# Optimization experiments

Hardware: AMD Instinct MI355X
Metric: run time of the kernel (lower is better)

Reference implementation:

```python
import jax, jax.numpy as jnp
import numpy as np

N_NODES = 100000
N_EDGES = 1600000
DIM = 128
N_BUNDLES = 8
BUNDLE_DIM = 4
HIDDEN = 256
TIME = 2


def setup_inputs() -> dict:
    key = jax.random.key(0)
    ks = jax.random.split(key, 8)
    x = jax.random.normal(ks[0], (N_NODES, DIM), dtype=jnp.float32)
    node_rep = jax.random.normal(ks[1], (N_NODES, N_BUNDLES, BUNDLE_DIM, BUNDLE_DIM), dtype=jnp.float32)
    # edge list; ensure every node has out-degree >= 1 so degree norm is finite
    src_extra = jax.random.randint(ks[2], (N_EDGES - N_NODES,), 0, N_NODES)
    src = jnp.concatenate([jnp.arange(N_NODES), src_extra]).astype(jnp.int64)
    dst = jax.random.randint(ks[3], (N_EDGES,), 0, N_NODES).astype(jnp.int64)
    w1 = jax.random.normal(ks[4], (HIDDEN, DIM), dtype=jnp.float32) * (1.0 / np.sqrt(DIM))
    b1 = jnp.zeros((HIDDEN,), dtype=jnp.float32)
    w2 = jax.random.normal(ks[5], (DIM, HIDDEN), dtype=jnp.float32) * (1.0 / np.sqrt(HIDDEN))
    b2 = jnp.zeros((DIM,), dtype=jnp.float32)
    return {"x": x, "node_rep": node_rep, "src": src, "dst": dst,
            "w1": w1, "b1": b1, "w2": w2, "b2": b2}


def reference(x, node_rep, src, dst, w1, b1, w2, b2):
    n = x.shape[0]
    # out-degrees (number of edges with node as source)
    deg = jax.ops.segment_sum(jnp.ones_like(src, dtype=x.dtype), src, num_segments=n)
    # u_mul_v: per-edge product of src and dst degrees -> symmetric norm coefs
    norm_coefs = jax.lax.rsqrt(deg[src] * deg[dst])  # [E]
    # per-bundle rotation: einsum('abcd,abde->abce', node_rep, vf)
    vf = x.reshape(n, N_BUNDLES, BUNDLE_DIM, -1)
    vf = jnp.einsum('nbcd,nbde->nbce', node_rep, vf)
    h = vf.reshape(n, DIM)
    # u_mul_e_sum repeated `time` times: out[dst] += h[src] * coef
    for _ in range(TIME):
        h = jax.ops.segment_sum(h[src] * norm_coefs[:, None], dst, num_segments=n)
    # inverse rotation with transposed node_rep
    vf = h.reshape(n, N_BUNDLES, BUNDLE_DIM, -1)
    vf = jnp.einsum('nbdc,nbde->nbce', node_rep, vf)
    h = vf.reshape(n, DIM)
    # feed-forward (dropout=0, exact GELU as in torch nn.GELU default)
    h = jax.nn.gelu(h @ w1.T + b1, approximate=False)
    return h @ w2.T + b2
```

## Files before the change

kernel.cpp:

```cpp
#include <hip/hip_runtime.h>
#include <hip/hip_bf16.h>
#include <math.h>

#define DIM 128
#define HID 256

typedef short s8x __attribute__((ext_vector_type(8)));
typedef float f4x __attribute__((ext_vector_type(4)));

__device__ __forceinline__ unsigned short f2bf(float f) {
    unsigned int u = __float_as_uint(f);
    u += 0x7FFF + ((u >> 16) & 1);
    return (unsigned short)(u >> 16);
}
__device__ __forceinline__ float bf2f(unsigned short b) {
    return __uint_as_float(((unsigned int)b) << 16);
}
__device__ __forceinline__ float bflo(unsigned int p) {
    return __uint_as_float(p << 16);
}
__device__ __forceinline__ float bfhi(unsigned int p) {
    return __uint_as_float(p & 0xffff0000u);
}


__global__ __launch_bounds__(256) void hist_kernel(
        const int* __restrict__ src, const int* __restrict__ dst,
        int* __restrict__ TD, int* __restrict__ TS, int nE, int nbuck, int chunk) {
    __shared__ int hd[1024], hs[1024];
    const int tid = threadIdx.x, blk = blockIdx.x;
    for (int b = tid; b < nbuck; b += 256) { hd[b] = 0; hs[b] = 0; }
    __syncthreads();
    int beg = blk * chunk, end = min(beg + chunk, nE);
    for (int i = beg + tid; i < end; i += 256) {
        atomicAdd(&hd[dst[i] >> 7], 1);
        atomicAdd(&hs[src[i] >> 7], 1);
    }
    __syncthreads();
    for (int b = tid; b < nbuck; b += 256) {
        TD[b * 256 + blk] = hd[b];
        TS[b * 256 + blk] = hs[b];
    }
}

__global__ void scan_blocks(const int* in, int* out, int* bsums, int n) {
    __shared__ int part[256];
    const int tid = threadIdx.x;
    const int base = blockIdx.x * 1024 + tid * 4;
    int v[4];
    int sum = 0;
#pragma unroll
    for (int k = 0; k < 4; ++k) {
        v[k] = (base + k < n) ? in[base + k] : 0;
        sum += v[k];
    }
    part[tid] = sum;
    __syncthreads();
    for (int off = 1; off < 256; off <<= 1) {
        int t = (tid >= off) ? part[tid - off] : 0;
        __syncthreads();
        part[tid] += t;
        __syncthreads();
    }
    int excl = part[tid] - sum;
    if (tid == 255) bsums[blockIdx.x] = part[255];
#pragma unroll
    for (int k = 0; k < 4; ++k) {
        if (base + k < n) out[base + k] = excl;
        excl += v[k];
    }
}

__global__ void scan_sums(int* bsums, int nb) {
    __shared__ int part[256];
    const int tid = threadIdx.x;
    const int base = tid * 4;
    int v[4];
    int sum = 0;
#pragma unroll
    for (int k = 0; k < 4; ++k) {
        v[k] = (base + k < nb) ? bsums[base + k] : 0;
        sum += v[k];
    }
    part[tid] = sum;
    __syncthreads();
    for (int off = 1; off < 256; off <<= 1) {
        int t = (tid >= off) ? part[tid - off] : 0;
        __syncthreads();
        part[tid] += t;
        __syncthreads();
    }
    int excl = part[tid] - sum;
#pragma unroll
    for (int k = 0; k < 4; ++k) {
        if (base + k < nb) bsums[base + k] = excl;
        excl += v[k];
    }
}

__global__ void scan_add(int* T, const int* __restrict__ bsums, int n2, int half, int E) {
    int i = blockIdx.x * blockDim.x + threadIdx.x;
    if (i < n2) {
        int v = T[i] + bsums[i >> 10];
        T[i] = (i >= half) ? v - E : v;
    }
}

__global__ __launch_bounds__(256) void scatter_edges(
        const int* __restrict__ src, const int* __restrict__ dst,
        const int* __restrict__ TD, const int* __restrict__ TS,
        unsigned long long* __restrict__ pairs, int* __restrict__ srcval,
        int nE, int nbuck, int chunk) {
    __shared__ int cd[1024], cs[1024];
    const int tid = threadIdx.x, blk = blockIdx.x;
    for (int b = tid; b < nbuck; b += 256) {
        cd[b] = TD[b * 256 + blk];
        cs[b] = TS[b * 256 + blk];
    }
    __syncthreads();
    int beg = blk * chunk, end = min(beg + chunk, nE);
    for (int i = beg + tid; i < end; i += 256) {
        int s = src[i], d = dst[i];
        int pd = atomicAdd(&cd[d >> 7], 1);
        pairs[pd] = ((unsigned long long)(unsigned)s << 32) | (unsigned)d;
        int ps = atomicAdd(&cs[s >> 7], 1);
        srcval[ps] = s;
    }
}

__global__ __launch_bounds__(256) void finalize_kernel(
        const unsigned long long* __restrict__ pairs, const int* __restrict__ TD,
        const int* __restrict__ srcval, const int* __restrict__ TS,
        int* __restrict__ rowstart, int* __restrict__ esrc,
        float* __restrict__ rdeg, int nE, int nbuck, int nN) {
    __shared__ int hist[128], sbuf[128], cur[128];
    const int tid = threadIdx.x, b = blockIdx.x;
    int beg = TD[b * 256];
    int end = (b + 1 < nbuck) ? TD[(b + 1) * 256] : nE;
    if (tid < 128) hist[tid] = 0;
    __syncthreads();
    for (int i = beg + tid; i < end; i += 256)
        atomicAdd(&hist[(int)((unsigned)pairs[i] & 127u)], 1);
    __syncthreads();
    int v = (tid < 128) ? hist[tid] : 0;
    if (tid < 128) sbuf[tid] = v;
    __syncthreads();
    for (int off = 1; off < 128; off <<= 1) {
        int t = (tid < 128 && tid >= off) ? sbuf[tid - off] : 0;
        __syncthreads();
        if (tid < 128) sbuf[tid] += t;
        __syncthreads();
    }
    if (tid < 128) {
        int excl = sbuf[tid] - v;
        cur[tid] = excl;
        int idx = (b << 7) + tid;
        if (idx <= nN) rowstart[idx] = beg + excl;
    }
    __syncthreads();
    for (int i = beg + tid; i < end; i += 256) {
        unsigned long long p = pairs[i];
        int l = (int)((unsigned)p & 127u);
        int s = (int)(p >> 32);
        int pos = atomicAdd(&cur[l], 1);
        esrc[beg + pos] = s;
    }
    __syncthreads();
    if (tid < 128) hist[tid] = 0;
    __syncthreads();
    int beg2 = TS[b * 256];
    int end2 = (b + 1 < nbuck) ? TS[(b + 1) * 256] : nE;
    for (int i = beg2 + tid; i < end2; i += 256)
        atomicAdd(&hist[srcval[i] & 127], 1);
    __syncthreads();
    if (tid < 128) {
        int idx = (b << 7) + tid;
        if (idx < nN) rdeg[idx] = rsqrtf((float)hist[tid]);
    }
}

__global__ void rot_cvt_kernel(const float* __restrict__ x, const float* __restrict__ R,
                               unsigned short* __restrict__ h0,
                               const float* __restrict__ w1, const float* __restrict__ w2,
                               unsigned short* __restrict__ w1b, unsigned short* __restrict__ w2b,
                               int n, int nbRot) {
    if ((int)blockIdx.x >= nbRot) {
        int t = (blockIdx.x - nbRot) * 256 + threadIdx.x;
        for (int i = t; i < 32768; i += 4096) {
            w1b[i] = f2bf(w1[i]);
            w2b[i] = f2bf(w2[i]);
        }
        return;
    }
    int u = blockIdx.x * blockDim.x + threadIdx.x;
    if (u >= n * 8) return;
    int nd = u >> 3, b = u & 7;
    const float* xp = &x[(size_t)nd * DIM + b * 16];
    const float* Rp = &R[(size_t)nd * DIM + b * 16];
    float xv[16], rv[16];
#pragma unroll
    for (int d = 0; d < 4; ++d) {
        *(float4*)&xv[d * 4] = *(const float4*)&xp[d * 4];
        *(float4*)&rv[d * 4] = *(const float4*)&Rp[d * 4];
    }
    unsigned short ob[16];
#pragma unroll
    for (int c = 0; c < 4; ++c)
#pragma unroll
        for (int e = 0; e < 4; ++e) {
            float acc = 0.f;
#pragma unroll
            for (int d = 0; d < 4; ++d) acc += rv[c * 4 + d] * xv[d * 4 + e];
            ob[c * 4 + e] = f2bf(acc);
        }
    unsigned short* op = &h0[(size_t)nd * DIM + b * 16];
    *(s8x*)&op[0] = *(s8x*)&ob[0];
    *(s8x*)&op[8] = *(s8x*)&ob[8];
}

__global__ __launch_bounds__(256) void gather_kernel(
        const unsigned short* __restrict__ hsrc, const int* __restrict__ esrc,
        const float* __restrict__ rdeg, const int* __restrict__ rowstart,
        unsigned short* __restrict__ hdst, int n) {
    int node = blockIdx.x * 8 + (threadIdx.x >> 5);
    int lane = threadIdx.x & 31;
    if (node >= n) return;
    int beg = rowstart[node];
    int end = rowstart[node + 1];
    float rd = rdeg[node];
    float a0 = 0.f, a1 = 0.f, a2 = 0.f, a3 = 0.f;
    int i = beg;
    for (; i + 2 <= end; i += 2) {
        int s0 = esrc[i], s1 = esrc[i + 1];
        float c0 = rdeg[s0] * rd;
        float c1 = rdeg[s1] * rd;
        uint2 p0 = *(const uint2*)&hsrc[(size_t)s0 * DIM + lane * 4];
        uint2 p1 = *(const uint2*)&hsrc[(size_t)s1 * DIM + lane * 4];
        a0 += bflo(p0.x) * c0 + bflo(p1.x) * c1;
        a1 += bfhi(p0.x) * c0 + bfhi(p1.x) * c1;
        a2 += bflo(p0.y) * c0 + bflo(p1.y) * c1;
        a3 += bfhi(p0.y) * c0 + bfhi(p1.y) * c1;
    }
    if (i < end) {
        int s0 = esrc[i];
        float c0 = rdeg[s0] * rd;
        uint2 p0 = *(const uint2*)&hsrc[(size_t)s0 * DIM + lane * 4];
        a0 += bflo(p0.x) * c0;
        a1 += bfhi(p0.x) * c0;
        a2 += bflo(p0.y) * c0;
        a3 += bfhi(p0.y) * c0;
    }
    uint2 packed;
    packed.x = (unsigned int)f2bf(a0) | ((unsigned int)f2bf(a1) << 16);
    packed.y = (unsigned int)f2bf(a2) | ((unsigned int)f2bf(a3) << 16);
    *(uint2*)&hdst[(size_t)node * DIM + lane * 4] = packed;
}

#define ABST 136
#define HBST 264
__global__ __launch_bounds__(256, 3) void ffn_kernel(
        const unsigned short* __restrict__ h,
        const float* __restrict__ R,
        const unsigned short* __restrict__ w1b,
        const float* __restrict__ b1,
        const unsigned short* __restrict__ w2b,
        const float* __restrict__ b2,
        float* __restrict__ out, int n) {
    __shared__ unsigned short abuf[64 * ABST];
    __shared__ unsigned short hbuf[64 * HBST];
    const int tid  = threadIdx.x;
    const int node0 = blockIdx.x * 64;
    const int wave = tid >> 6;
    const int lane = tid & 63;
    const int lr = lane & 15;
    const int lq = lane >> 4;

    for (int u = tid; u < 512; u += 256) {
        int nd = u >> 3, b = u & 7;
        int gn = node0 + nd;
        float hv[16], rv[16];
        if (gn < n) {
            const unsigned short* hp = &h[(size_t)gn * DIM + b * 16];
            const float* Rp = &R[(size_t)gn * DIM + b * 16];
            unsigned short hraw[16];
            *(s8x*)&hraw[0] = *(const s8x*)&hp[0];
            *(s8x*)&hraw[8] = *(const s8x*)&hp[8];
#pragma unroll
            for (int d = 0; d < 16; ++d) hv[d] = bf2f(hraw[d]);
#pragma unroll
            for (int d = 0; d < 4; ++d)
                *(float4*)&rv[d * 4] = *(const float4*)&Rp[d * 4];
        } else {
#pragma unroll
            for (int d = 0; d < 16; ++d) { hv[d] = 0.f; rv[d] = 0.f; }
        }
#pragma unroll
        for (int c = 0; c < 4; ++c) {
            unsigned short gb[4];
#pragma unroll
            for (int e = 0; e < 4; ++e) {
                float acc = 0.f;
#pragma unroll
                for (int d = 0; d < 4; ++d) acc += rv[d * 4 + c] * hv[d * 4 + e];
                gb[e] = f2bf(acc);
            }
            *(ushort4*)&abuf[nd * ABST + b * 16 + c * 4] =
                make_ushort4(gb[0], gb[1], gb[2], gb[3]);
        }
    }
    __syncthreads();

    f4x acc1[4][4];
#pragma unroll
    for (int mt = 0; mt < 4; ++mt)
#pragma unroll
        for (int nt = 0; nt < 4; ++nt) acc1[mt][nt] = (f4x){0.f, 0.f, 0.f, 0.f};

    const int nw = wave * 64;
    for (int ks = 0; ks < 4; ++ks) {
        const int k0 = ks * 32 + lq * 8;
        s8x af[4], bf[4];
#pragma unroll
        for (int mt = 0; mt < 4; ++mt)
            af[mt] = *(const s8x*)&abuf[(mt * 16 + lr) * ABST + k0];
#pragma unroll
        for (int nt = 0; nt < 4; ++nt)
            bf[nt] = *(const s8x*)&w1b[(size_t)(nw + nt * 16 + lr) * 128 + k0];
#pragma unroll
        for (int mt = 0; mt < 4; ++mt)
#pragma unroll
            for (int nt = 0; nt < 4; ++nt)
                acc1[mt][nt] = __builtin_amdgcn_mfma_f32_16x16x32_bf16(
                    af[mt], bf[nt], acc1[mt][nt], 0, 0, 0);
    }
#pragma unroll
    for (int nt = 0; nt < 4; ++nt) {
        int nn = nw + nt * 16 + lr;
        float bias = b1[nn];
#pragma unroll
        for (int mt = 0; mt < 4; ++mt) {
#pragma unroll
            for (int r = 0; r < 4; ++r) {
                float v = acc1[mt][nt][r] + bias;
                v = 0.5f * v * (1.f + erff(v * 0.70710678118654752f));
                hbuf[(mt * 16 + lq * 4 + r) * HBST + nn] = f2bf(v);
            }
        }
    }
    __syncthreads();

    f4x acc2[4][2];
#pragma unroll
    for (int mt = 0; mt < 4; ++mt)
#pragma unroll
        for (int nt = 0; nt < 2; ++nt) acc2[mt][nt] = (f4x){0.f, 0.f, 0.f, 0.f};

    const int nw2 = wave * 32;
    for (int ks = 0; ks < 8; ++ks) {
        const int k0 = ks * 32 + lq * 8;
        s8x af[4], bf2v[2];
#pragma unroll
        for (int mt = 0; mt < 4; ++mt)
            af[mt] = *(const s8x*)&hbuf[(mt * 16 + lr) * HBST + k0];
#pragma unroll
        for (int nt = 0; nt < 2; ++nt)
            bf2v[nt] = *(const s8x*)&w2b[(size_t)(nw2 + nt * 16 + lr) * 256 + k0];
#pragma unroll
        for (int mt = 0; mt < 4; ++mt)
#pragma unroll
            for (int nt = 0; nt < 2; ++nt)
                acc2[mt][nt] = __builtin_amdgcn_mfma_f32_16x16x32_bf16(
                    af[mt], bf2v[nt], acc2[mt][nt], 0, 0, 0);
    }
#pragma unroll
    for (int nt = 0; nt < 2; ++nt) {
        int n2 = nw2 + nt * 16 + lr;
        float bias = b2[n2];
#pragma unroll
        for (int mt = 0; mt < 4; ++mt) {
#pragma unroll
            for (int r = 0; r < 4; ++r) {
                int gn = node0 + mt * 16 + lq * 4 + r;
                if (gn < n) out[(size_t)gn * DIM + n2] = acc2[mt][nt][r] + bias;
            }
        }
    }
}

extern "C" void kernel_launch(void* const* d_in, const int* in_sizes, int n_in,
                              void* d_out, int out_size, void* d_ws, size_t ws_size,
                              hipStream_t stream) {
    const float* x   = (const float*)d_in[0];
    const float* R   = (const float*)d_in[1];
    const int*   src = (const int*)d_in[2];
    const int*   dst = (const int*)d_in[3];
    const float* w1  = (const float*)d_in[4];
    const float* b1  = (const float*)d_in[5];
    const float* w2  = (const float*)d_in[6];
    const float* b2  = (const float*)d_in[7];
    float* out = (float*)d_out;

    const int N = in_sizes[0] / DIM;
    const int E = in_sizes[2];

    const int nbuck = (N + 127) >> 7;
    const int chunk = (E + 255) / 256;
    const int nScan = nbuck * 256;
    const int nScan2 = 2 * nScan;
    const int nbScan2 = (nScan2 + 1023) / 1024;

    unsigned short* hA = (unsigned short*)d_ws;
    unsigned short* hM = hA + (size_t)N * DIM;
    unsigned long long* pairs = (unsigned long long*)hM;
    int* srcval = (int*)(pairs + E);
    float* rdeg     = (float*)(hM + (size_t)N * DIM);
    int*   rowstart = (int*)(rdeg + N);
    int*   esrc     = rowstart + (N + 1);
    int*   TD       = esrc + E;
    int*   TS       = TD + nScan;
    int*   bsums    = TS + nScan;
    unsigned short* w1b = (unsigned short*)(bsums + 1024);
    unsigned short* w2b = w1b + 32768;

    const int BLK = 256;

    hist_kernel<<<256, BLK, 0, stream>>>(src, dst, TD, TS, E, nbuck, chunk);
    scan_blocks<<<nbScan2, BLK, 0, stream>>>(TD, TD, bsums, nScan2);
    scan_sums<<<1, BLK, 0, stream>>>(bsums, nbScan2);
    scan_add<<<(nScan2 + BLK - 1) / BLK, BLK, 0, stream>>>(TD, bsums, nScan2, nScan, E);
    scatter_edges<<<256, BLK, 0, stream>>>(src, dst, TD, TS, pairs, srcval, E, nbuck, chunk);
    finalize_kernel<<<nbuck, BLK, 0, stream>>>(pairs, TD, srcval, TS, rowstart, esrc, rdeg, E, nbuck, N);

    const int nbRot = ((size_t)N * 8 + BLK - 1) / BLK;
    rot_cvt_kernel<<<nbRot + 16, BLK, 0, stream>>>(x, R, hA, w1, w2, w1b, w2b, N, nbRot);

    gather_kernel<<<(N + 7) / 8, BLK, 0, stream>>>(hA, esrc, rdeg, rowstart, hM, N);
    gather_kernel<<<(N + 7) / 8, BLK, 0, stream>>>(hM, esrc, rdeg, rowstart, hA, N);

    ffn_kernel<<<(N + 63) / 64, BLK, 0, stream>>>(hA, R, w1b, b1, w2b, b2, out, N);
}
```

Measured before the change: 444.0 us.

## Replace bucketed CSR build with atomic counting sort and pack edge coefficients

Replaces the two-level bucketed histogram/scatter/finalize CSR construction with per-node global atomic degree counts, one scan, and an atomic-cursor scatter. It also stores (src, precomputed norm coefficient) pairs per edge so the gather skips the rdeg lookup. The gather now uses 16 lanes per node with 16-byte loads, and the FFN shares one LDS buffer between its two stages to allow 4 blocks per CU. Global atomics on random node ids may contend, and the edge order within a row becomes nondeterministic.

New measurement: 554.2 us. 24.8% more time.

```diff
diff --git a/kernel.cpp b/kernel.cpp
--- a/kernel.cpp
+++ b/kernel.cpp
@@ -24,22 +24,22 @@
 }
 
 
-__global__ __launch_bounds__(256) void hist_kernel(
+__global__ void prep_kernel(const float* __restrict__ w1, const float* __restrict__ w2,
+                            unsigned short* __restrict__ w1b, unsigned short* __restrict__ w2b,
+                            int* __restrict__ outdeg, int* __restrict__ rowcnt, int nN) {
+    const int t = blockIdx.x * 256 + threadIdx.x;
+    w1b[t] = f2bf(w1[t]);
+    w2b[t] = f2bf(w2[t]);
+    for (int i = t; i < nN; i += 32768) { outdeg[i] = 0; rowcnt[i] = 0; }
+}
+
+__global__ __launch_bounds__(256) void count_kernel(
         const int* __restrict__ src, const int* __restrict__ dst,
-        int* __restrict__ TD, int* __restrict__ TS, int nE, int nbuck, int chunk) {
-    __shared__ int hd[1024], hs[1024];
-    const int tid = threadIdx.x, blk = blockIdx.x;
-    for (int b = tid; b < nbuck; b += 256) { hd[b] = 0; hs[b] = 0; }
-    __syncthreads();
-    int beg = blk * chunk, end = min(beg + chunk, nE);
-    for (int i = beg + tid; i < end; i += 256) {
-        atomicAdd(&hd[dst[i] >> 7], 1);
-        atomicAdd(&hs[src[i] >> 7], 1);
-    }
-    __syncthreads();
-    for (int b = tid; b < nbuck; b += 256) {
-        TD[b * 256 + blk] = hd[b];
-        TS[b * 256 + blk] = hs[b];
+        int* __restrict__ outdeg, int* __restrict__ rowcnt, int nE) {
+    int i = blockIdx.x * 256 + threadIdx.x;
+    if (i < nE) {
+        atomicAdd(&outdeg[src[i]], 1);
+        atomicAdd(&rowcnt[dst[i]], 1);
     }
 }
 
@@ -98,100 +98,37 @@
     }
 }
 
-__global__ void scan_add(int* T, const int* __restrict__ bsums, int n2, int half, int E) {
+__global__ void scan_add(int* __restrict__ rowstart, const int* __restrict__ bsums,
+                         int* __restrict__ cursor, const int* __restrict__ outdeg,
+                         float* __restrict__ rdeg, int nN, int E) {
     int i = blockIdx.x * blockDim.x + threadIdx.x;
-    if (i < n2) {
-        int v = T[i] + bsums[i >> 10];
-        T[i] = (i >= half) ? v - E : v;
-    }
-}
-
-__global__ __launch_bounds__(256) void scatter_edges(
+    if (i < nN) {
+        int v = rowstart[i] + bsums[i >> 10];
+        rowstart[i] = v;
+        cursor[i] = v;
+        rdeg[i] = rsqrtf((float)outdeg[i]);
+    }
+    if (i == 0) rowstart[nN] = E;
+}
+
+template<bool PACK>
+__global__ __launch_bounds__(256) void scatter_kernel(
         const int* __restrict__ src, const int* __restrict__ dst,
-        const int* __restrict__ TD, const int* __restrict__ TS,
-        unsigned long long* __restrict__ pairs, int* __restrict__ srcval,
-        int nE, int nbuck, int chunk) {
-    __shared__ int cd[1024], cs[1024];
-    const int tid = threadIdx.x, blk = blockIdx.x;
-    for (int b = tid; b < nbuck; b += 256) {
-        cd[b] = TD[b * 256 + blk];
-        cs[b] = TS[b * 256 + blk];
-    }
-    __syncthreads();
-    int beg = blk * chunk, end = min(beg + chunk, nE);
-    for (int i = beg + tid; i < end; i += 256) {
-        int s = src[i], d = dst[i];
-        int pd = atomicAdd(&cd[d >> 7], 1);
-        pairs[pd] = ((unsigned long long)(unsigned)s << 32) | (unsigned)d;
-        int ps = atomicAdd(&cs[s >> 7], 1);
-        srcval[ps] = s;
-    }
-}
-
-__global__ __launch_bounds__(256) void finalize_kernel(
-        const unsigned long long* __restrict__ pairs, const int* __restrict__ TD,
-        const int* __restrict__ srcval, const int* __restrict__ TS,
-        int* __restrict__ rowstart, int* __restrict__ esrc,
-        float* __restrict__ rdeg, int nE, int nbuck, int nN) {
-    __shared__ int hist[128], sbuf[128], cur[128];
-    const int tid = threadIdx.x, b = blockIdx.x;
-    int beg = TD[b * 256];
-    int end = (b + 1 < nbuck) ? TD[(b + 1) * 256] : nE;
-    if (tid < 128) hist[tid] = 0;
-    __syncthreads();
-    for (int i = beg + tid; i < end; i += 256)
-        atomicAdd(&hist[(int)((unsigned)pairs[i] & 127u)], 1);
-    __syncthreads();
-    int v = (tid < 128) ? hist[tid] : 0;
-    if (tid < 128) sbuf[tid] = v;
-    __syncthreads();
-    for (int off = 1; off < 128; off <<= 1) {
-        int t = (tid < 128 && tid >= off) ? sbuf[tid - off] : 0;
-        __syncthreads();
-        if (tid < 128) sbuf[tid] += t;
-        __syncthreads();
-    }
-    if (tid < 128) {
-        int excl = sbuf[tid] - v;
-        cur[tid] = excl;
-        int idx = (b << 7) + tid;
-        if (idx <= nN) rowstart[idx] = beg + excl;
-    }
-    __syncthreads();
-    for (int i = beg + tid; i < end; i += 256) {
-        unsigned long long p = pairs[i];
-        int l = (int)((unsigned)p & 127u);
-        int s = (int)(p >> 32);
-        int pos = atomicAdd(&cur[l], 1);
-        esrc[beg + pos] = s;
-    }
-    __syncthreads();
-    if (tid < 128) hist[tid] = 0;
-    __syncthreads();
-    int beg2 = TS[b * 256];
-    int end2 = (b + 1 < nbuck) ? TS[(b + 1) * 256] : nE;
-    for (int i = beg2 + tid; i < end2; i += 256)
-        atomicAdd(&hist[srcval[i] & 127], 1);
-    __syncthreads();
-    if (tid < 128) {
-        int idx = (b << 7) + tid;
-        if (idx < nN) rdeg[idx] = rsqrtf((float)hist[tid]);
+        int* __restrict__ cursor, const float* __restrict__ rdeg,
+        uint2* __restrict__ ecsr, int* __restrict__ esrcA, int nE) {
+    int i = blockIdx.x * 256 + threadIdx.x;
+    if (i >= nE) return;
+    int s = src[i], d = dst[i];
+    int pos = atomicAdd(&cursor[d], 1);
+    if (PACK) {
+        ecsr[pos] = make_uint2((unsigned)s, __float_as_uint(rdeg[s] * rdeg[d]));
+    } else {
+        esrcA[pos] = s;
     }
 }
 
 __global__ void rot_cvt_kernel(const float* __restrict__ x, const float* __restrict__ R,
-                               unsigned short* __restrict__ h0,
-                               const float* __restrict__ w1, const float* __restrict__ w2,
-                               unsigned short* __restrict__ w1b, unsigned short* __restrict__ w2b,
-                               int n, int nbRot) {
-    if ((int)blockIdx.x >= nbRot) {
-        int t = (blockIdx.x - nbRot) * 256 + threadIdx.x;
-        for (int i = t; i < 32768; i += 4096) {
-            w1b[i] = f2bf(w1[i]);
-            w2b[i] = f2bf(w2[i]);
-        }
-        return;
-    }
+                               unsigned short* __restrict__ h0, int n) {
     int u = blockIdx.x * blockDim.x + threadIdx.x;
     if (u >= n * 8) return;
     int nd = u >> 3, b = u & 7;
@@ -218,47 +155,75 @@
     *(s8x*)&op[8] = *(s8x*)&ob[8];
 }
 
+template<bool PACK>
 __global__ __launch_bounds__(256) void gather_kernel(
-        const unsigned short* __restrict__ hsrc, const int* __restrict__ esrc,
+        const unsigned short* __restrict__ hsrc,
+        const uint2* __restrict__ ecsr, const int* __restrict__ esrcA,
         const float* __restrict__ rdeg, const int* __restrict__ rowstart,
         unsigned short* __restrict__ hdst, int n) {
-    int node = blockIdx.x * 8 + (threadIdx.x >> 5);
-    int lane = threadIdx.x & 31;
+    const int node = blockIdx.x * 16 + (threadIdx.x >> 4);
+    const int lane = threadIdx.x & 15;
     if (node >= n) return;
-    int beg = rowstart[node];
-    int end = rowstart[node + 1];
-    float rd = rdeg[node];
+    const int beg = rowstart[node];
+    const int end = rowstart[node + 1];
+    float rd = 0.f;
+    if (!PACK) rd = rdeg[node];
     float a0 = 0.f, a1 = 0.f, a2 = 0.f, a3 = 0.f;
+    float a4 = 0.f, a5 = 0.f, a6 = 0.f, a7 = 0.f;
     int i = beg;
     for (; i + 2 <= end; i += 2) {
-        int s0 = esrc[i], s1 = esrc[i + 1];
-        float c0 = rdeg[s0] * rd;
-        float c1 = rdeg[s1] * rd;
-        uint2 p0 = *(const uint2*)&hsrc[(size_t)s0 * DIM + lane * 4];
-        uint2 p1 = *(const uint2*)&hsrc[(size_t)s1 * DIM + lane * 4];
+        int s0, s1;
+        float c0, c1;
+        if (PACK) {
+            uint2 e0 = ecsr[i], e1 = ecsr[i + 1];
+            s0 = (int)e0.x; c0 = __uint_as_float(e0.y);
+            s1 = (int)e1.x; c1 = __uint_as_float(e1.y);
+        } else {
+            s0 = esrcA[i]; s1 = esrcA[i + 1];
+            c0 = rdeg[s0] * rd; c1 = rdeg[s1] * rd;
+        }
+        uint4 p0 = *(const uint4*)&hsrc[(size_t)s0 * DIM + lane * 8];
+        uint4 p1 = *(const uint4*)&hsrc[(size_t)s1 * DIM + lane * 8];
         a0 += bflo(p0.x) * c0 + bflo(p1.x) * c1;
         a1 += bfhi(p0.x) * c0 + bfhi(p1.x) * c1;
         a2 += bflo(p0.y) * c0 + bflo(p1.y) * c1;
         a3 += bfhi(p0.y) * c0 + bfhi(p1.y) * c1;
+        a4 += bflo(p0.z) * c0 + bflo(p1.z) * c1;
+        a5 += bfhi(p0.z) * c0 + bfhi(p1.z) * c1;
+        a6 += bflo(p0.w) * c0 + bflo(p1.w) * c1;
+        a7 += bfhi(p0.w) * c0 + bfhi(p1.w) * c1;
     }
     if (i < end) {
-        int s0 = esrc[i];
-        float c0 = rdeg[s0] * rd;
-        uint2 p0 = *(const uint2*)&hsrc[(size_t)s0 * DIM + lane * 4];
+        int s0;
+        float c0;
+        if (PACK) {
+            uint2 e0 = ecsr[i];
+            s0 = (int)e0.x; c0 = __uint_as_float(e0.y);
+        } else {
+            s0 = esrcA[i];
+            c0 = rdeg[s0] * rd;
+        }
+        uint4 p0 = *(const uint4*)&hsrc[(size_t)s0 * DIM + lane * 8];
         a0 += bflo(p0.x) * c0;
         a1 += bfhi(p0.x) * c0;
         a2 += bflo(p0.y) * c0;
         a3 += bfhi(p0.y) * c0;
-    }
-    uint2 packed;
-    packed.x = (unsigned int)f2bf(a0) | ((unsigned int)f2bf(a1) << 16);
-    packed.y = (unsigned int)f2bf(a2) | ((unsigned int)f2bf(a3) << 16);
-    *(uint2*)&hdst[(size_t)node * DIM + lane * 4] = packed;
+        a4 += bflo(p0.z) * c0;
+        a5 += bfhi(p0.z) * c0;
+        a6 += bflo(p0.w) * c0;
+        a7 += bfhi(p0.w) * c0;
+    }
+    uint4 o;
+    o.x = (unsigned)f2bf(a0) | ((unsigned)f2bf(a1) << 16);
+    o.y = (unsigned)f2bf(a2) | ((unsigned)f2bf(a3) << 16);
+    o.z = (unsigned)f2bf(a4) | ((unsigned)f2bf(a5) << 16);
+    o.w = (unsigned)f2bf(a6) | ((unsigned)f2bf(a7) << 16);
+    *(uint4*)&hdst[(size_t)node * DIM + lane * 8] = o;
 }
 
 #define ABST 136
 #define HBST 264
-__global__ __launch_bounds__(256, 3) void ffn_kernel(
+__global__ __launch_bounds__(256, 4) void ffn_kernel(
         const unsigned short* __restrict__ h,
         const float* __restrict__ R,
         const unsigned short* __restrict__ w1b,
@@ -266,8 +231,9 @@
         const unsigned short* __restrict__ w2b,
         const float* __restrict__ b2,
         float* __restrict__ out, int n) {
-    __shared__ unsigned short abuf[64 * ABST];
-    __shared__ unsigned short hbuf[64 * HBST];
+    __shared__ unsigned short smem[64 * HBST];
+    unsigned short* abuf = smem;
+    unsigned short* hbuf = smem;
     const int tid  = threadIdx.x;
     const int node0 = blockIdx.x * 64;
     const int wave = tid >> 6;
@@ -319,20 +285,22 @@
     const int nw = wave * 64;
     for (int ks = 0; ks < 4; ++ks) {
         const int k0 = ks * 32 + lq * 8;
-        s8x af[4], bf[4];
+        s8x af[4], bfv[4];
 #pragma unroll
         for (int mt = 0; mt < 4; ++mt)
             af[mt] = *(const s8x*)&abuf[(mt * 16 + lr) * ABST + k0];
 #pragma unroll
         for (int nt = 0; nt < 4; ++nt)
-            bf[nt] = *(const s8x*)&w1b[(size_t)(nw + nt * 16 + lr) * 128 + k0];
+            bfv[nt] = *(const s8x*)&w1b[(size_t)(nw + nt * 16 + lr) * 128 + k0];
 #pragma unroll
         for (int mt = 0; mt < 4; ++mt)
 #pragma unroll
             for (int nt = 0; nt < 4; ++nt)
                 acc1[mt][nt] = __builtin_amdgcn_mfma_f32_16x16x32_bf16(
-                    af[mt], bf[nt], acc1[mt][nt], 0, 0, 0);
-    }
+                    af[mt], bfv[nt], acc1[mt][nt], 0, 0, 0);
+    }
+    __syncthreads();
+
 #pragma unroll
     for (int nt = 0; nt < 4; ++nt) {
         int nn = nw + nt * 16 + lr;
@@ -403,39 +371,61 @@
     const int N = in_sizes[0] / DIM;
     const int E = in_sizes[2];
 
-    const int nbuck = (N + 127) >> 7;
-    const int chunk = (E + 255) / 256;
-    const int nScan = nbuck * 256;
-    const int nScan2 = 2 * nScan;
-    const int nbScan2 = (nScan2 + 1023) / 1024;
-
     unsigned short* hA = (unsigned short*)d_ws;
     unsigned short* hM = hA + (size_t)N * DIM;
-    unsigned long long* pairs = (unsigned long long*)hM;
-    int* srcval = (int*)(pairs + E);
-    float* rdeg     = (float*)(hM + (size_t)N * DIM);
-    int*   rowstart = (int*)(rdeg + N);
-    int*   esrc     = rowstart + (N + 1);
-    int*   TD       = esrc + E;
-    int*   TS       = TD + nScan;
-    int*   bsums    = TS + nScan;
+    char* edge_base = (char*)(hM + (size_t)N * DIM);
+    const size_t tail_bytes = (size_t)N * 4 * 3 + (size_t)(N + 1) * 4 +
+                              1024 * 4 + 2 * 32768 * 2;
+    const size_t fixed_bytes = (size_t)N * DIM * 4;
+    const bool use_pack =
+        (fixed_bytes + (size_t)E * 8 + tail_bytes) <= ws_size;
+    const size_t edge_bytes = use_pack ? (size_t)E * 8 : (size_t)E * 4;
+
+    uint2* ecsr = (uint2*)edge_base;
+    int*   esrcA = (int*)edge_base;
+    char* q = edge_base + edge_bytes;
+    float* rdeg     = (float*)q;
+    int*   outdeg   = (int*)(rdeg + N);
+    int*   rowcnt   = outdeg + N;
+    int*   rowstart = rowcnt + N;
+    int*   bsums    = rowstart + (N + 1);
     unsigned short* w1b = (unsigned short*)(bsums + 1024);
     unsigned short* w2b = w1b + 32768;
+    int* cursor = rowcnt;
 
     const int BLK = 256;
-
-    hist_kernel<<<256, BLK, 0, stream>>>(src, dst, TD, TS, E, nbuck, chunk);
-    scan_blocks<<<nbScan2, BLK, 0, stream>>>(TD, TD, bsums, nScan2);
-    scan_sums<<<1, BLK, 0, stream>>>(bsums, nbScan2);
-    scan_add<<<(nScan2 + BLK - 1) / BLK, BLK, 0, stream>>>(TD, bsums, nScan2, nScan, E);
-    scatter_edges<<<256, BLK, 0, stream>>>(src, dst, TD, TS, pairs, srcval, E, nbuck, chunk);
-    finalize_kernel<<<nbuck, BLK, 0, stream>>>(pairs, TD, srcval, TS, rowstart, esrc, rdeg, E, nbuck, N);
+    const int nbScan = (N + 1023) / 1024;
+    const int nbE = (E + BLK - 1) / BLK;
+
+    prep_kernel<<<128, BLK, 0, stream>>>(w1, w2, w1b, w2b, outdeg, rowcnt, N);
+
+    count_kernel<<<nbE, BLK, 0, stream>>>(src, dst, outdeg, rowcnt, E);
+    scan_blocks<<<nbScan, BLK, 0, stream>>>(rowcnt, rowstart, bsums, N);
+    scan_sums<<<1, BLK, 0, stream>>>(bsums, nbScan);
+    scan_add<<<(N + BLK - 1) / BLK, BLK, 0, stream>>>(rowstart, bsums, cursor,
+                                                      outdeg, rdeg, N, E);
+    if (use_pack)
+        scatter_kernel<true><<<nbE, BLK, 0, stream>>>(src, dst, cursor, rdeg,
+                                                      ecsr, esrcA, E);
+    else
+        scatter_kernel<false><<<nbE, BLK, 0, stream>>>(src, dst, cursor, rdeg,
+                                                       ecsr, esrcA, E);
 
     const int nbRot = ((size_t)N * 8 + BLK - 1) / BLK;
-    rot_cvt_kernel<<<nbRot + 16, BLK, 0, stream>>>(x, R, hA, w1, w2, w1b, w2b, N, nbRot);
-
-    gather_kernel<<<(N + 7) / 8, BLK, 0, stream>>>(hA, esrc, rdeg, rowstart, hM, N);
-    gather_kernel<<<(N + 7) / 8, BLK, 0, stream>>>(hM, esrc, rdeg, rowstart, hA, N);
+    rot_cvt_kernel<<<nbRot, BLK, 0, stream>>>(x, R, hA, N);
+
+    const int nbG = (N + 15) / 16;
+    if (use_pack) {
+        gather_kernel<true><<<nbG, BLK, 0, stream>>>(hA, ecsr, esrcA, rdeg,
+                                                     rowstart, hM, N);
+        gather_kernel<true><<<nbG, BLK, 0, stream>>>(hM, ecsr, esrcA, rdeg,
+                                                     rowstart, hA, N);
+    } else {
+        gather_kernel<false><<<nbG, BLK, 0, stream>>>(hA, ecsr, esrcA, rdeg,
+                                                      rowstart, hM, N);
+        gather_kernel<false><<<nbG, BLK, 0, stream>>>(hM, ecsr, esrcA, rdeg,
+                                                      rowstart, hA, N);
+    }
 
     ffn_kernel<<<(N + 63) / 64, BLK, 0, stream>>>(hA, R, w1b, b1, w2b, b2, out, N);
 }
```

## Compact edge buffers, precompute edge coefficients, widen gather loads, shrink FFN LDS

Applied to the files above, without the earlier changes.

Scatter now writes 32-bit packed (src<<7|dst_lo) pairs and a single byte per source entry, where it used to write 64-bit pairs and 32-bit source values. The old finalize kernel is split into a source-degree pass and a destination CSR pass. When the workspace is large enough, that pass stores (src, coef) pairs so the gathers skip the random rdeg lookups. The gather uses 16 lanes per node with 16-byte loads, and the FFN kernel aliases its two LDS buffers (adding a barrier) so it can raise launch bounds to 4 blocks. This trades an extra kernel launch and 8-byte edge reads for less scattered traffic, and relies on the workspace-size check.

Result: faster. 430.7 us (-3.0%).

```diff
diff --git a/kernel.cpp b/kernel.cpp
--- a/kernel.cpp
+++ b/kernel.cpp
@@ -109,7 +109,7 @@
 __global__ __launch_bounds__(256) void scatter_edges(
         const int* __restrict__ src, const int* __restrict__ dst,
         const int* __restrict__ TD, const int* __restrict__ TS,
-        unsigned long long* __restrict__ pairs, int* __restrict__ srcval,
+        unsigned int* __restrict__ pairs, unsigned char* __restrict__ sbyte,
         int nE, int nbuck, int chunk) {
     __shared__ int cd[1024], cs[1024];
     const int tid = threadIdx.x, blk = blockIdx.x;
@@ -122,17 +122,36 @@
     for (int i = beg + tid; i < end; i += 256) {
         int s = src[i], d = dst[i];
         int pd = atomicAdd(&cd[d >> 7], 1);
-        pairs[pd] = ((unsigned long long)(unsigned)s << 32) | (unsigned)d;
+        pairs[pd] = ((unsigned)s << 7) | (unsigned)(d & 127);
         int ps = atomicAdd(&cs[s >> 7], 1);
-        srcval[ps] = s;
-    }
-}
-
-__global__ __launch_bounds__(256) void finalize_kernel(
-        const unsigned long long* __restrict__ pairs, const int* __restrict__ TD,
-        const int* __restrict__ srcval, const int* __restrict__ TS,
-        int* __restrict__ rowstart, int* __restrict__ esrc,
+        sbyte[ps] = (unsigned char)(s & 127);
+    }
+}
+
+__global__ __launch_bounds__(256) void finalize_src(
+        const unsigned char* __restrict__ sbyte, const int* __restrict__ TS,
         float* __restrict__ rdeg, int nE, int nbuck, int nN) {
+    __shared__ int hist[128];
+    const int tid = threadIdx.x, b = blockIdx.x;
+    if (tid < 128) hist[tid] = 0;
+    __syncthreads();
+    int beg = TS[b * 256];
+    int end = (b + 1 < nbuck) ? TS[(b + 1) * 256] : nE;
+    for (int i = beg + tid; i < end; i += 256)
+        atomicAdd(&hist[sbyte[i]], 1);
+    __syncthreads();
+    if (tid < 128) {
+        int idx = (b << 7) + tid;
+        if (idx < nN) rdeg[idx] = rsqrtf((float)hist[tid]);
+    }
+}
+
+template<bool PACK>
+__global__ __launch_bounds__(256) void finalize_dst(
+        const unsigned int* __restrict__ pairs, const int* __restrict__ TD,
+        const float* __restrict__ rdeg,
+        int* __restrict__ rowstart, uint2* __restrict__ ecsr,
+        int* __restrict__ esrcA, int nE, int nbuck, int nN) {
     __shared__ int hist[128], sbuf[128], cur[128];
     const int tid = threadIdx.x, b = blockIdx.x;
     int beg = TD[b * 256];
@@ -140,7 +159,7 @@
     if (tid < 128) hist[tid] = 0;
     __syncthreads();
     for (int i = beg + tid; i < end; i += 256)
-        atomicAdd(&hist[(int)((unsigned)pairs[i] & 127u)], 1);
+        atomicAdd(&hist[(int)(pairs[i] & 127u)], 1);
     __syncthreads();
     int v = (tid < 128) ? hist[tid] : 0;
     if (tid < 128) sbuf[tid] = v;
@@ -159,23 +178,16 @@
     }
     __syncthreads();
     for (int i = beg + tid; i < end; i += 256) {
-        unsigned long long p = pairs[i];
-        int l = (int)((unsigned)p & 127u);
-        int s = (int)(p >> 32);
+        unsigned int p = pairs[i];
+        int l = (int)(p & 127u);
+        int s = (int)(p >> 7);
         int pos = atomicAdd(&cur[l], 1);
-        esrc[beg + pos] = s;
-    }
-    __syncthreads();
-    if (tid < 128) hist[tid] = 0;
-    __syncthreads();
-    int beg2 = TS[b * 256];
-    int end2 = (b + 1 < nbuck) ? TS[(b + 1) * 256] : nE;
-    for (int i = beg2 + tid; i < end2; i += 256)
-        atomicAdd(&hist[srcval[i] & 127], 1);
-    __syncthreads();
-    if (tid < 128) {
-        int idx = (b << 7) + tid;
-        if (idx < nN) rdeg[idx] = rsqrtf((float)hist[tid]);
+        if (PACK) {
+            float coef = rdeg[s] * rdeg[(b << 7) + l];
+            ecsr[beg + pos] = make_uint2((unsigned)s, __float_as_uint(coef));
+        } else {
+            esrcA[beg + pos] = s;
+        }
     }
 }
 
@@ -218,47 +230,75 @@
     *(s8x*)&op[8] = *(s8x*)&ob[8];
 }
 
+template<bool PACK>
 __global__ __launch_bounds__(256) void gather_kernel(
-        const unsigned short* __restrict__ hsrc, const int* __restrict__ esrc,
+        const unsigned short* __restrict__ hsrc,
+        const uint2* __restrict__ ecsr, const int* __restrict__ esrcA,
         const float* __restrict__ rdeg, const int* __restrict__ rowstart,
         unsigned short* __restrict__ hdst, int n) {
-    int node = blockIdx.x * 8 + (threadIdx.x >> 5);
-    int lane = threadIdx.x & 31;
+    const int node = blockIdx.x * 16 + (threadIdx.x >> 4);
+    const int lane = threadIdx.x & 15;
     if (node >= n) return;
-    int beg = rowstart[node];
-    int end = rowstart[node + 1];
-    float rd = rdeg[node];
+    const int beg = rowstart[node];
+    const int end = rowstart[node + 1];
+    float rd = 0.f;
+    if (!PACK) rd = rdeg[node];
     float a0 = 0.f, a1 = 0.f, a2 = 0.f, a3 = 0.f;
+    float a4 = 0.f, a5 = 0.f, a6 = 0.f, a7 = 0.f;
     int i = beg;
     for (; i + 2 <= end; i += 2) {
-        int s0 = esrc[i], s1 = esrc[i + 1];
-        float c0 = rdeg[s0] * rd;
-        float c1 = rdeg[s1] * rd;
-        uint2 p0 = *(const uint2*)&hsrc[(size_t)s0 * DIM + lane * 4];
-        uint2 p1 = *(const uint2*)&hsrc[(size_t)s1 * DIM + lane * 4];
+        int s0, s1;
+        float c0, c1;
+        if (PACK) {
+            uint2 e0 = ecsr[i], e1 = ecsr[i + 1];
+            s0 = (int)e0.x; c0 = __uint_as_float(e0.y);
+            s1 = (int)e1.x; c1 = __uint_as_float(e1.y);
+        } else {
+            s0 = esrcA[i]; s1 = esrcA[i + 1];
+            c0 = rdeg[s0] * rd; c1 = rdeg[s1] * rd;
+        }
+        uint4 p0 = *(const uint4*)&hsrc[(size_t)s0 * DIM + lane * 8];
+        uint4 p1 = *(const uint4*)&hsrc[(size_t)s1 * DIM + lane * 8];
         a0 += bflo(p0.x) * c0 + bflo(p1.x) * c1;
         a1 += bfhi(p0.x) * c0 + bfhi(p1.x) * c1;
         a2 += bflo(p0.y) * c0 + bflo(p1.y) * c1;
         a3 += bfhi(p0.y) * c0 + bfhi(p1.y) * c1;
+        a4 += bflo(p0.z) * c0 + bflo(p1.z) * c1;
+        a5 += bfhi(p0.z) * c0 + bfhi(p1.z) * c1;
+        a6 += bflo(p0.w) * c0 + bflo(p1.w) * c1;
+        a7 += bfhi(p0.w) * c0 + bfhi(p1.w) * c1;
     }
     if (i < end) {
-        int s0 = esrc[i];
-        float c0 = rdeg[s0] * rd;
-        uint2 p0 = *(const uint2*)&hsrc[(size_t)s0 * DIM + lane * 4];
+        int s0;
+        float c0;
+        if (PACK) {
+            uint2 e0 = ecsr[i];
+            s0 = (int)e0.x; c0 = __uint_as_float(e0.y);
+        } else {
+            s0 = esrcA[i];
+            c0 = rdeg[s0] * rd;
+        }
+        uint4 p0 = *(const uint4*)&hsrc[(size_t)s0 * DIM + lane * 8];
         a0 += bflo(p0.x) * c0;
         a1 += bfhi(p0.x) * c0;
         a2 += bflo(p0.y) * c0;
         a3 += bfhi(p0.y) * c0;
-    }
-    uint2 packed;
-    packed.x = (unsigned int)f2bf(a0) | ((unsigned int)f2bf(a1) << 16);
-    packed.y = (unsigned int)f2bf(a2) | ((unsigned int)f2bf(a3) << 16);
-    *(uint2*)&hdst[(size_t)node * DIM + lane * 4] = packed;
+        a4 += bflo(p0.z) * c0;
+        a5 += bfhi(p0.z) * c0;
+        a6 += bflo(p0.w) * c0;
+        a7 += bfhi(p0.w) * c0;
+    }
+    uint4 o;
+    o.x = (unsigned)f2bf(a0) | ((unsigned)f2bf(a1) << 16);
+    o.y = (unsigned)f2bf(a2) | ((unsigned)f2bf(a3) << 16);
+    o.z = (unsigned)f2bf(a4) | ((unsigned)f2bf(a5) << 16);
+    o.w = (unsigned)f2bf(a6) | ((unsigned)f2bf(a7) << 16);
+    *(uint4*)&hdst[(size_t)node * DIM + lane * 8] = o;
 }
 
 #define ABST 136
 #define HBST 264
-__global__ __launch_bounds__(256, 3) void ffn_kernel(
+__global__ __launch_bounds__(256, 4) void ffn_kernel(
         const unsigned short* __restrict__ h,
         const float* __restrict__ R,
         const unsigned short* __restrict__ w1b,
@@ -266,8 +306,9 @@
         const unsigned short* __restrict__ w2b,
         const float* __restrict__ b2,
         float* __restrict__ out, int n) {
-    __shared__ unsigned short abuf[64 * ABST];
-    __shared__ unsigned short hbuf[64 * HBST];
+    __shared__ unsigned short smem[64 * HBST];
+    unsigned short* abuf = smem;
+    unsigned short* hbuf = smem;
     const int tid  = threadIdx.x;
     const int node0 = blockIdx.x * 64;
     const int wave = tid >> 6;
@@ -319,20 +360,22 @@
     const int nw = wave * 64;
     for (int ks = 0; ks < 4; ++ks) {
         const int k0 = ks * 32 + lq * 8;
-        s8x af[4], bf[4];
+        s8x af[4], bfv[4];
 #pragma unroll
         for (int mt = 0; mt < 4; ++mt)
             af[mt] = *(const s8x*)&abuf[(mt * 16 + lr) * ABST + k0];
 #pragma unroll
         for (int nt = 0; nt < 4; ++nt)
-            bf[nt] = *(const s8x*)&w1b[(size_t)(nw + nt * 16 + lr) * 128 + k0];
+            bfv[nt] = *(const s8x*)&w1b[(size_t)(nw + nt * 16 + lr) * 128 + k0];
 #pragma unroll
         for (int mt = 0; mt < 4; ++mt)
 #pragma unroll
             for (int nt = 0; nt < 4; ++nt)
                 acc1[mt][nt] = __builtin_amdgcn_mfma_f32_16x16x32_bf16(
-                    af[mt], bf[nt], acc1[mt][nt], 0, 0, 0);
-    }
+                    af[mt], bfv[nt], acc1[mt][nt], 0, 0, 0);
+    }
+    __syncthreads();
+
 #pragma unroll
     for (int nt = 0; nt < 4; ++nt) {
         int nn = nw + nt * 16 + lr;
@@ -411,12 +454,22 @@
 
     unsigned short* hA = (unsigned short*)d_ws;
     unsigned short* hM = hA + (size_t)N * DIM;
-    unsigned long long* pairs = (unsigned long long*)hM;
-    int* srcval = (int*)(pairs + E);
-    float* rdeg     = (float*)(hM + (size_t)N * DIM);
+    unsigned int*  pairs = (unsigned int*)hM;
+    unsigned char* sbyte = (unsigned char*)(pairs + E);
+    char* edge_base = (char*)(hM + (size_t)N * DIM);
+
+    const size_t tail_bytes = (size_t)N * 4 + (size_t)(N + 1) * 4 +
+                              (size_t)nScan * 8 + 1024 * 4 + 2 * 32768 * 2;
+    const size_t fixed_bytes = (size_t)N * DIM * 4;
+    const bool use_pack = (fixed_bytes + (size_t)E * 8 + tail_bytes) <= ws_size;
+    const size_t edge_bytes = use_pack ? (size_t)E * 8 : (size_t)E * 4;
+
+    uint2* ecsr  = (uint2*)edge_base;
+    int*   esrcA = (int*)edge_base;
+    char* q = edge_base + edge_bytes;
+    float* rdeg     = (float*)q;
     int*   rowstart = (int*)(rdeg + N);
-    int*   esrc     = rowstart + (N + 1);
-    int*   TD       = esrc + E;
+    int*   TD       = rowstart + (N + 1);
     int*   TS       = TD + nScan;
     int*   bsums    = TS + nScan;
     unsigned short* w1b = (unsigned short*)(bsums + 1024);
@@ -428,14 +481,30 @@
     scan_blocks<<<nbScan2, BLK, 0, stream>>>(TD, TD, bsums, nScan2);
     scan_sums<<<1, BLK, 0, stream>>>(bsums, nbScan2);
     scan_add<<<(nScan2 + BLK - 1) / BLK, BLK, 0, stream>>>(TD, bsums, nScan2, nScan, E);
-    scatter_edges<<<256, BLK, 0, stream>>>(src, dst, TD, TS, pairs, srcval, E, nbuck, chunk);
-    finalize_kernel<<<nbuck, BLK, 0, stream>>>(pairs, TD, srcval, TS, rowstart, esrc, rdeg, E, nbuck, N);
+    scatter_edges<<<256, BLK, 0, stream>>>(src, dst, TD, TS, pairs, sbyte, E, nbuck, chunk);
+    finalize_src<<<nbuck, BLK, 0, stream>>>(sbyte, TS, rdeg, E, nbuck, N);
+    if (use_pack)
+        finalize_dst<true><<<nbuck, BLK, 0, stream>>>(pairs, TD, rdeg, rowstart,
+                                                      ecsr, esrcA, E, nbuck, N);
+    else
+        finalize_dst<false><<<nbuck, BLK, 0, stream>>>(pairs, TD, rdeg, rowstart,
+                                                       ecsr, esrcA, E, nbuck, N);
 
     const int nbRot = ((size_t)N * 8 + BLK - 1) / BLK;
     rot_cvt_kernel<<<nbRot + 16, BLK, 0, stream>>>(x, R, hA, w1, w2, w1b, w2b, N, nbRot);
 
-    gather_kernel<<<(N + 7) / 8, BLK, 0, stream>>>(hA, esrc, rdeg, rowstart, hM, N);
-    gather_kernel<<<(N + 7) / 8, BLK, 0, stream>>>(hM, esrc, rdeg, rowstart, hA, N);
+    const int nbG = (N + 15) / 16;
+    if (use_pack) {
+        gather_kernel<true><<<nbG, BLK, 0, stream>>>(hA, ecsr, esrcA, rdeg,
+                                                     rowstart, hM, N);
+        gather_kernel<true><<<nbG, BLK, 0, stream>>>(hM, ecsr, esrcA, rdeg,
+                                                     rowstart, hA, N);
+    } else {
+        gather_kernel<false><<<nbG, BLK, 0, stream>>>(hA, ecsr, esrcA, rdeg,
+                                                      rowstart, hM, N);
+        gather_kernel<false><<<nbG, BLK, 0, stream>>>(hM, ecsr, esrcA, rdeg,
+                                                      rowstart, hA, N);
+    }
 
     ffn_kernel<<<(N + 63) / 64, BLK, 0, stream>>>(hA, R, w1b, b1, w2b, b2, out, N);
 }
```
